# Kernel tuning notes

Measured on AMD Instinct MI355X. Metric: run time of the kernel, lower is better.

Reference implementation:

```python
import jax, jax.numpy as jnp
import numpy as np

B, S, H = 32, 2048, 1024

def setup_inputs() -> dict:
    key = jax.random.key(0)
    ks = jax.random.split(key, 8)
    sc = 1.0 / np.sqrt(H)
    return {
        "decoder_hidden": jax.random.normal(ks[0], (B, H), jnp.float32),
        "encoder_outputs": jax.random.normal(ks[1], (B, S, H), jnp.float32),
        "mask": jax.random.randint(ks[2], (B, S), 0, 2, jnp.int32),
        "Wa_w": jax.random.normal(ks[3], (H, H), jnp.float32) * sc,
        "Wa_b": jax.random.normal(ks[4], (H,), jnp.float32) * sc,
        "Ua_w": jax.random.normal(ks[5], (H, H), jnp.float32) * sc,
        "Ua_b": jax.random.normal(ks[6], (H,), jnp.float32) * sc,
        "Va_w": jax.random.normal(ks[7], (H,), jnp.float32) * sc,
        "Va_b": jnp.float32(0.0),
    }

def reference(decoder_hidden, encoder_outputs, mask, Wa_w, Wa_b, Ua_w, Ua_b, Va_w, Va_b):
    # dec proj: [B,H] -> [B,1,H]; enc proj: [B,S,H]
    dec_proj = (decoder_hidden @ Wa_w + Wa_b)[:, None, :]
    enc_proj = jnp.einsum('bsh,hk->bsk', encoder_outputs, Ua_w) + Ua_b
    energy = jnp.tanh(dec_proj + enc_proj)                      # [B,S,H]
    scores = jnp.einsum('bsh,h->bs', energy, Va_w) + Va_b       # [B,S]
    scores = jnp.where(mask == 0, jnp.float32(-1e9), scores)
    return jax.nn.softmax(scores, axis=1)
```

## Files before the change

### kernel.cpp

```cpp
#include <hip/hip_runtime.h>
#include <math.h>

#define BB 32
#define SS 2048
#define HH 1024
#define MT (BB*SS)

#define BM 256
#define BN 256
#define BK 32
#define NT (HH/BK)
#define NCH (HH/BN)
#define THREADS 512
#define BTILE 16384

typedef float  f32x4 __attribute__((ext_vector_type(4)));
typedef short  s16x8 __attribute__((ext_vector_type(8)));
typedef unsigned short u16;

__device__ inline void split1(float x, u16& h, u16& l) {
    unsigned u = __float_as_uint(x);
    h = (u16)(u >> 16);
    float hf = __uint_as_float((u >> 16) << 16);
    l = (u16)(__float_as_uint(x - hf) >> 16);
}
__device__ inline void split8v(float4 v0, float4 v1, s16x8& h, s16x8& l) {
    float x[8] = {v0.x,v0.y,v0.z,v0.w,v1.x,v1.y,v1.z,v1.w};
    #pragma unroll
    for (int j = 0; j < 8; ++j) {
        u16 hh, ll; split1(x[j], hh, ll);
        h[j] = (short)hh; l[j] = (short)ll;
    }
}

__device__ __forceinline__ void gload16(const u16* g, u16* l) {
    __builtin_amdgcn_global_load_lds(
        (const __attribute__((address_space(1))) unsigned int*)g,
        (__attribute__((address_space(3))) unsigned int*)l, 16, 0, 0);
}

__global__ void dec_proj_kernel(const float* __restrict__ dh,
                                const float* __restrict__ Wa_w,
                                const float* __restrict__ Wa_b,
                                const float* __restrict__ Ua_b,
                                float* __restrict__ dec_proj) {
    __shared__ float sdh[HH];
    const int b   = blockIdx.x;
    const int nq  = blockIdx.y;
    const int tid = threadIdx.x;
    for (int i = tid; i < HH; i += 256) sdh[i] = dh[b*HH + i];
    __syncthreads();
    const int n = nq*256 + tid;
    float acc = Wa_b[n] + Ua_b[n];
    for (int k = 0; k < HH; ++k)
        acc = fmaf(sdh[k], Wa_w[(size_t)k*HH + n], acc);
    dec_proj[b*HH + n] = acc;
}

__global__ void transpose_convert_kernel(const float* __restrict__ Ua,
                                         u16* __restrict__ B_pre) {
    __shared__ u16 shh[64][72], shl[64][72];
    const int nb = blockIdx.x * 64, kb = blockIdx.y * 64;
    const int tid = threadIdx.x;
    const int kl = tid >> 4, nl4 = (tid & 15) * 4;
    #pragma unroll
    for (int q = 0; q < 4; ++q) {
        const int k = kl + q*16;
        float4 v = *(const float4*)&Ua[(size_t)(kb + k)*HH + nb + nl4];
        float x[4] = {v.x, v.y, v.z, v.w};
        #pragma unroll
        for (int j = 0; j < 4; ++j) {
            u16 hh, ll; split1(x[j], hh, ll);
            shh[k][nl4 + j] = hh; shl[k][nl4 + j] = ll;
        }
    }
    __syncthreads();
    const int nl = tid >> 3, kc8 = (tid & 7) * 8;
    #pragma unroll
    for (int q = 0; q < 2; ++q) {
        const int n = nb + nl + q*32;
        const int kglob = kb + kc8;
        s16x8 hv, lv;
        #pragma unroll
        for (int j = 0; j < 8; ++j) {
            hv[j] = (short)shh[kc8 + j][nl + q*32];
            lv[j] = (short)shl[kc8 + j][nl + q*32];
        }
        const int nchI = n >> 8, fI = (n >> 4) & 15, lrI = n & 15;
        const int ktI = kglob >> 5, cI = (kglob >> 3) & 3;
        const size_t base = (size_t)(nchI*32 + ktI) * BTILE;
        const size_t idxH = base + fI*512 + (cI*16 + lrI)*8;
        *(s16x8*)&B_pre[idxH]        = hv;
        *(s16x8*)&B_pre[idxH + 8192] = lv;
    }
}

__global__ __launch_bounds__(THREADS, 1)
void gemm_fr_kernel(const float* __restrict__ A,
                    const u16* __restrict__ B_pre,
                    const float* __restrict__ dec_proj,
                    const float* __restrict__ Va_w,
                    float* __restrict__ partials)
{
    __shared__ __align__(16) u16 AhS[2][BM*BK];
    __shared__ __align__(16) u16 AlS[2][BM*BK];
    __shared__ __align__(16) u16 BS[2][BTILE];

    const int bid = blockIdx.x;
    const int wg  = (bid & 7) * 128 + (bid >> 3);
    const int nch = wg & 3;
    const int mt  = wg >> 2;
    const int m0  = mt * BM, n0 = nch * BN;

    const int tid = threadIdx.x, lane = tid & 63, wid = tid >> 6;
    const int wm = wid >> 2, wn = wid & 3;
    const int lr = lane & 15, lk = lane >> 4;

    const int srow = tid >> 1, shalf = tid & 1;
    const float* Ab = A + (size_t)(m0 + srow)*HH + shalf*16;
    const int awoff0 = (srow>>4)*512 + (shalf*2    )*128 + (srow&15)*8;
    const int awoff1 = (srow>>4)*512 + (shalf*2 + 1)*128 + (srow&15)*8;
    const u16* Btile = B_pre + (size_t)nch*NT*BTILE + wid*2048 + lane*8;

    f32x4 acc[8][4];
    #pragma unroll
    for (int i = 0; i < 8; ++i)
        #pragma unroll
        for (int j = 0; j < 4; ++j) acc[i][j] = (f32x4){0.f,0.f,0.f,0.f};

    s16x8  bh[4], bl[4];
    float4 a0_, a1_, a2_, a3_;

    auto gloadB = [&](int kt, int db) {
        const u16* src = Btile + (size_t)kt*BTILE;
        u16* dst = &BS[db][wid*2048];
        gload16(src,        dst);
        gload16(src +  512, dst +  512);
        gload16(src + 1024, dst + 1024);
        gload16(src + 1536, dst + 1536);
    };
    auto loadA = [&](int kt) {
        const float* p = Ab + kt*BK;
        a0_ = *(const float4*)(p + 0);
        a1_ = *(const float4*)(p + 4);
        a2_ = *(const float4*)(p + 8);
        a3_ = *(const float4*)(p + 12);
    };
    auto writeA = [&](int db) {
        s16x8 h, l;
        split8v(a0_, a1_, h, l);
        *(s16x8*)&AhS[db][awoff0] = h; *(s16x8*)&AlS[db][awoff0] = l;
        split8v(a2_, a3_, h, l);
        *(s16x8*)&AhS[db][awoff1] = h; *(s16x8*)&AlS[db][awoff1] = l;
    };
    auto readB = [&](int cb) {
        #pragma unroll
        for (int j = 0; j < 4; ++j) {
            const int off = (wn*4 + j)*512 + lane*8;
            bh[j] = *(const s16x8*)&BS[cb][off];
            bl[j] = *(const s16x8*)&BS[cb][8192 + off];
        }
    };

    loadA(0);
    gloadB(0, 0);
    writeA(0);
    __syncthreads();
    loadA(1);

    for (int j = 0; j < NT; ++j) {
        const int cb = j & 1;
        const bool hn = (j + 1 < NT);
        if (hn) gloadB(j + 1, cb ^ 1);
        __builtin_amdgcn_sched_barrier(0);

        readB(cb);
        s16x8 ahp[2], alp[2];
        {   const int o = (wm*8 + 0)*512 + lane*8;
            ahp[0] = *(const s16x8*)&AhS[cb][o];
            alp[0] = *(const s16x8*)&AlS[cb][o]; }
        #pragma unroll
        for (int f = 0; f < 8; ++f) {
            if (f < 7) {
                const int o = (wm*8 + f + 1)*512 + lane*8;
                ahp[(f+1)&1] = *(const s16x8*)&AhS[cb][o];
                alp[(f+1)&1] = *(const s16x8*)&AlS[cb][o];
            }
            const s16x8 ah = ahp[f&1], al = alp[f&1];
            __builtin_amdgcn_s_setprio(1);
            #pragma unroll
            for (int q = 0; q < 4; ++q) {
                f32x4 c = acc[f][q];
                c = __builtin_amdgcn_mfma_f32_16x16x32_bf16(ah, bh[q], c, 0, 0, 0);
                c = __builtin_amdgcn_mfma_f32_16x16x32_bf16(ah, bl[q], c, 0, 0, 0);
                c = __builtin_amdgcn_mfma_f32_16x16x32_bf16(al, bh[q], c, 0, 0, 0);
                acc[f][q] = c;
            }
            __builtin_amdgcn_s_setprio(0);
        }
        if (hn) {
            writeA(cb ^ 1);
            loadA(j + 2 < NT ? j + 2 : j + 1);
        }
        __syncthreads();
    }

    const int bidx = m0 >> 11;
    float dp[4], va[4];
    #pragma unroll
    for (int j = 0; j < 4; ++j) {
        const int n = n0 + wn*64 + j*16 + lr;
        dp[j] = dec_proj[bidx*HH + n];
        va[j] = Va_w[n];
    }
    #pragma unroll
    for (int i = 0; i < 8; ++i) {
        #pragma unroll
        for (int r = 0; r < 4; ++r) {
            float s = 0.f;
            #pragma unroll
            for (int j = 0; j < 4; ++j)
                s += va[j] * tanhf(acc[i][j][r] + dp[j]);
            s += __shfl_xor(s, 1, 64);
            s += __shfl_xor(s, 2, 64);
            s += __shfl_xor(s, 4, 64);
            s += __shfl_xor(s, 8, 64);
            if (lr == 0) {
                const int m = m0 + wm*128 + i*16 + lk*4 + r;
                partials[(size_t)m*16 + nch*4 + wn] = s;
            }
        }
    }
}

__global__ void softmax_kernel(const float* __restrict__ partials,
                               const int* __restrict__ mask,
                               const float* __restrict__ vb_ptr,
                               float* __restrict__ out)
{
    const int b   = blockIdx.x;
    const int tid = threadIdx.x;
    __shared__ float sred[8];
    const float vb = vb_ptr[0];
    float sc[8];
    float mymax = -INFINITY;
    #pragma unroll
    for (int i = 0; i < 8; ++i) {
        const int s = i*256 + tid;
        const float4* p = (const float4*)&partials[((size_t)b*SS + s)*16];
        const float4 x = p[0], y = p[1], z = p[2], w = p[3];
        float v = (((x.x+x.y)+(x.z+x.w)) + ((y.x+y.y)+(y.z+y.w)))
                + (((z.x+z.y)+(z.z+z.w)) + ((w.x+w.y)+(w.z+w.w))) + vb;
        if (mask[b*SS + s] == 0) v = -1e9f;
        sc[i] = v;
        mymax = fmaxf(mymax, v);
    }
    #pragma unroll
    for (int off = 1; off < 64; off <<= 1)
        mymax = fmaxf(mymax, __shfl_xor(mymax, off, 64));
    const int wave = tid >> 6, lane = tid & 63;
    if (lane == 0) sred[wave] = mymax;
    __syncthreads();
    const float bmax = fmaxf(fmaxf(sred[0], sred[1]), fmaxf(sred[2], sred[3]));
    float ex[8], mysum = 0.f;
    #pragma unroll
    for (int i = 0; i < 8; ++i) {
        ex[i] = __expf(sc[i] - bmax);
        mysum += ex[i];
    }
    #pragma unroll
    for (int off = 1; off < 64; off <<= 1)
        mysum += __shfl_xor(mysum, off, 64);
    if (lane == 0) sred[4 + wave] = mysum;
    __syncthreads();
    const float inv = 1.f / (sred[4] + sred[5] + sred[6] + sred[7]);
    #pragma unroll
    for (int i = 0; i < 8; ++i)
        out[(size_t)b*SS + i*256 + tid] = ex[i] * inv;
}

extern "C" void kernel_launch(void* const* d_in, const int* in_sizes, int n_in,
                              void* d_out, int out_size, void* d_ws, size_t ws_size,
                              hipStream_t stream) {
    const float* dh   = (const float*)d_in[0];
    const float* enc  = (const float*)d_in[1];
    const int*   mask = (const int*)d_in[2];
    const float* Wa_w = (const float*)d_in[3];
    const float* Wa_b = (const float*)d_in[4];
    const float* Ua_w = (const float*)d_in[5];
    const float* Ua_b = (const float*)d_in[6];
    const float* Va_w = (const float*)d_in[7];
    const float* Va_b = (const float*)d_in[8];
    float* out = (float*)d_out;

    float* dec_proj = (float*)d_ws;
    float* partials = dec_proj + BB*HH;
    u16*   B_pre    = (u16*)(partials + (size_t)MT*16);

    dec_proj_kernel<<<dim3(BB, 4), 256, 0, stream>>>(dh, Wa_w, Wa_b, Ua_b, dec_proj);
    transpose_convert_kernel<<<dim3(HH/64, HH/64), 256, 0, stream>>>(Ua_w, B_pre);
    gemm_fr_kernel<<<(MT/BM)*NCH, THREADS, 0, stream>>>(enc, B_pre, dec_proj, Va_w, partials);
    softmax_kernel<<<BB, 256, 0, stream>>>(partials, mask, Va_b, out);
}
```

Baseline: 418.7 us.

## Switch GEMM to 32x32x16 bf16 MFMA with matching LDS fragment layouts

Replaces the 16x16x32 bf16 MFMA tiling with 32x32x16 MFMA instructions and re-lays out the pre-split B buffer and the A shared-memory staging to match 32-wide fragments. The per-wave work is now 4x2 tiles of 32x32 with two k-substeps, and the epilogue reduction now spans 32 lanes. The larger MFMA shape is meant to cut the number of instructions issued and the LDS fragment reads per FLOP. In exchange the row-to-lane mapping and the accumulator layout are more involved, which raises the risk of indexing mistakes and of LDS bank conflicts.

```diff
diff --git a/kernel.cpp b/kernel.cpp
--- a/kernel.cpp
+++ b/kernel.cpp
@@ -14,8 +14,8 @@
 #define THREADS 512
 #define BTILE 16384
 
-typedef float  f32x4 __attribute__((ext_vector_type(4)));
-typedef short  s16x8 __attribute__((ext_vector_type(8)));
+typedef float  f32x16 __attribute__((ext_vector_type(16)));
+typedef short  s16x8  __attribute__((ext_vector_type(8)));
 typedef unsigned short u16;
 
 __device__ inline void split1(float x, u16& h, u16& l) {
@@ -86,10 +86,10 @@
             hv[j] = (short)shh[kc8 + j][nl + q*32];
             lv[j] = (short)shl[kc8 + j][nl + q*32];
         }
-        const int nchI = n >> 8, fI = (n >> 4) & 15, lrI = n & 15;
-        const int ktI = kglob >> 5, cI = (kglob >> 3) & 3;
-        const size_t base = (size_t)(nchI*32 + ktI) * BTILE;
-        const size_t idxH = base + fI*512 + (cI*16 + lrI)*8;
+        const int nchI = n >> 8, nfI = (n >> 5) & 7, colr = n & 31;
+        const int ktI = kglob >> 5, ksI = (kglob >> 4) & 1, chI = (kglob >> 3) & 1;
+        const size_t base = (size_t)(nchI*NT + ktI) * BTILE;
+        const size_t idxH = base + nfI*1024 + ksI*512 + colr*16 + chI*8;
         *(s16x8*)&B_pre[idxH]        = hv;
         *(s16x8*)&B_pre[idxH + 8192] = lv;
     }
@@ -114,21 +114,26 @@
 
     const int tid = threadIdx.x, lane = tid & 63, wid = tid >> 6;
     const int wm = wid >> 2, wn = wid & 3;
-    const int lr = lane & 15, lk = lane >> 4;
-
-    const int srow = tid >> 1, shalf = tid & 1;
-    const float* Ab = A + (size_t)(m0 + srow)*HH + shalf*16;
-    const int awoff0 = (srow>>4)*512 + (shalf*2    )*128 + (srow&15)*8;
-    const int awoff1 = (srow>>4)*512 + (shalf*2 + 1)*128 + (srow&15)*8;
+    const int lc = lane & 31, lh = lane >> 5;
+
+    const int e0 = tid, e1 = tid + 512;
+    const float* Ab0 = A + (size_t)(m0 + (e0>>7)*32 + ((e0>>1)&31))*HH
+                         + ((e0>>6)&1)*16 + (e0&1)*8;
+    const float* Ab1 = A + (size_t)(m0 + (e1>>7)*32 + ((e1>>1)&31))*HH
+                         + ((e1>>6)&1)*16 + (e1&1)*8;
+    const int aw0 = tid*8, aw1 = tid*8 + 4096;
     const u16* Btile = B_pre + (size_t)nch*NT*BTILE + wid*2048 + lane*8;
-
-    f32x4 acc[8][4];
-    #pragma unroll
-    for (int i = 0; i < 8; ++i)
-        #pragma unroll
-        for (int j = 0; j < 4; ++j) acc[i][j] = (f32x4){0.f,0.f,0.f,0.f};
-
-    s16x8  bh[4], bl[4];
+    const int laneoff = lc*16 + lh*8;
+
+    f32x16 acc[4][2];
+    #pragma unroll
+    for (int i = 0; i < 4; ++i)
+        #pragma unroll
+        for (int j = 0; j < 2; ++j)
+            #pragma unroll
+            for (int r = 0; r < 16; ++r) acc[i][j][r] = 0.f;
+
+    s16x8  bh[2][2], bl[2][2];
     float4 a0_, a1_, a2_, a3_;
 
     auto gloadB = [&](int kt, int db) {
@@ -140,26 +145,29 @@
         gload16(src + 1536, dst + 1536);
     };
     auto loadA = [&](int kt) {
-        const float* p = Ab + kt*BK;
-        a0_ = *(const float4*)(p + 0);
-        a1_ = *(const float4*)(p + 4);
-        a2_ = *(const float4*)(p + 8);
-        a3_ = *(const float4*)(p + 12);
+        const float* p0 = Ab0 + kt*BK;
+        const float* p1 = Ab1 + kt*BK;
+        a0_ = *(const float4*)(p0 + 0);
+        a1_ = *(const float4*)(p0 + 4);
+        a2_ = *(const float4*)(p1 + 0);
+        a3_ = *(const float4*)(p1 + 4);
     };
     auto writeA = [&](int db) {
         s16x8 h, l;
         split8v(a0_, a1_, h, l);
-        *(s16x8*)&AhS[db][awoff0] = h; *(s16x8*)&AlS[db][awoff0] = l;
+        *(s16x8*)&AhS[db][aw0] = h; *(s16x8*)&AlS[db][aw0] = l;
         split8v(a2_, a3_, h, l);
-        *(s16x8*)&AhS[db][awoff1] = h; *(s16x8*)&AlS[db][awoff1] = l;
+        *(s16x8*)&AhS[db][aw1] = h; *(s16x8*)&AlS[db][aw1] = l;
     };
     auto readB = [&](int cb) {
         #pragma unroll
-        for (int j = 0; j < 4; ++j) {
-            const int off = (wn*4 + j)*512 + lane*8;
-            bh[j] = *(const s16x8*)&BS[cb][off];
-            bl[j] = *(const s16x8*)&BS[cb][8192 + off];
-        }
+        for (int nf = 0; nf < 2; ++nf)
+            #pragma unroll
+            for (int ks = 0; ks < 2; ++ks) {
+                const int off = (wn*2 + nf)*1024 + ks*512 + laneoff;
+                bh[nf][ks] = *(const s16x8*)&BS[cb][off];
+                bl[nf][ks] = *(const s16x8*)&BS[cb][8192 + off];
+            }
     };
 
     loadA(0);
@@ -175,26 +183,34 @@
         __builtin_amdgcn_sched_barrier(0);
 
         readB(cb);
-        s16x8 ahp[2], alp[2];
-        {   const int o = (wm*8 + 0)*512 + lane*8;
-            ahp[0] = *(const s16x8*)&AhS[cb][o];
-            alp[0] = *(const s16x8*)&AlS[cb][o]; }
-        #pragma unroll
-        for (int f = 0; f < 8; ++f) {
-            if (f < 7) {
-                const int o = (wm*8 + f + 1)*512 + lane*8;
-                ahp[(f+1)&1] = *(const s16x8*)&AhS[cb][o];
-                alp[(f+1)&1] = *(const s16x8*)&AlS[cb][o];
+        s16x8 ahp[2][2], alp[2][2];
+        #pragma unroll
+        for (int ks = 0; ks < 2; ++ks) {
+            const int o = (wm*4 + 0)*1024 + ks*512 + laneoff;
+            ahp[0][ks] = *(const s16x8*)&AhS[cb][o];
+            alp[0][ks] = *(const s16x8*)&AlS[cb][o];
+        }
+        #pragma unroll
+        for (int mf = 0; mf < 4; ++mf) {
+            if (mf < 3) {
+                #pragma unroll
+                for (int ks = 0; ks < 2; ++ks) {
+                    const int o = (wm*4 + mf + 1)*1024 + ks*512 + laneoff;
+                    ahp[(mf+1)&1][ks] = *(const s16x8*)&AhS[cb][o];
+                    alp[(mf+1)&1][ks] = *(const s16x8*)&AlS[cb][o];
+                }
             }
-            const s16x8 ah = ahp[f&1], al = alp[f&1];
             __builtin_amdgcn_s_setprio(1);
             #pragma unroll
-            for (int q = 0; q < 4; ++q) {
-                f32x4 c = acc[f][q];
-                c = __builtin_amdgcn_mfma_f32_16x16x32_bf16(ah, bh[q], c, 0, 0, 0);
-                c = __builtin_amdgcn_mfma_f32_16x16x32_bf16(ah, bl[q], c, 0, 0, 0);
-                c = __builtin_amdgcn_mfma_f32_16x16x32_bf16(al, bh[q], c, 0, 0, 0);
-                acc[f][q] = c;
+            for (int nf = 0; nf < 2; ++nf) {
+                f32x16 c = acc[mf][nf];
+                #pragma unroll
+                for (int ks = 0; ks < 2; ++ks) {
+                    c = __builtin_amdgcn_mfma_f32_32x32x16_bf16(ahp[mf&1][ks], bh[nf][ks], c, 0, 0, 0);
+                    c = __builtin_amdgcn_mfma_f32_32x32x16_bf16(ahp[mf&1][ks], bl[nf][ks], c, 0, 0, 0);
+                    c = __builtin_amdgcn_mfma_f32_32x32x16_bf16(alp[mf&1][ks], bh[nf][ks], c, 0, 0, 0);
+                }
+                acc[mf][nf] = c;
             }
             __builtin_amdgcn_s_setprio(0);
         }
@@ -206,27 +222,26 @@
     }
 
     const int bidx = m0 >> 11;
-    float dp[4], va[4];
-    #pragma unroll
-    for (int j = 0; j < 4; ++j) {
-        const int n = n0 + wn*64 + j*16 + lr;
-        dp[j] = dec_proj[bidx*HH + n];
-        va[j] = Va_w[n];
-    }
-    #pragma unroll
-    for (int i = 0; i < 8; ++i) {
-        #pragma unroll
-        for (int r = 0; r < 4; ++r) {
-            float s = 0.f;
-            #pragma unroll
-            for (int j = 0; j < 4; ++j)
-                s += va[j] * tanhf(acc[i][j][r] + dp[j]);
+    float dp2[2], va2[2];
+    #pragma unroll
+    for (int nf = 0; nf < 2; ++nf) {
+        const int n = n0 + wn*64 + nf*32 + lc;
+        dp2[nf] = dec_proj[bidx*HH + n];
+        va2[nf] = Va_w[n];
+    }
+    #pragma unroll
+    for (int mf = 0; mf < 4; ++mf) {
+        #pragma unroll
+        for (int r = 0; r < 16; ++r) {
+            float s = va2[0] * tanhf(acc[mf][0][r] + dp2[0])
+                    + va2[1] * tanhf(acc[mf][1][r] + dp2[1]);
             s += __shfl_xor(s, 1, 64);
             s += __shfl_xor(s, 2, 64);
             s += __shfl_xor(s, 4, 64);
             s += __shfl_xor(s, 8, 64);
-            if (lr == 0) {
-                const int m = m0 + wm*128 + i*16 + lk*4 + r;
+            s += __shfl_xor(s, 16, 64);
+            if (lc == 0) {
+                const int m = m0 + wm*128 + mf*32 + (r & 3) + 8*(r >> 2) + 4*lh;
                 partials[(size_t)m*16 + nch*4 + wn] = s;
             }
         }
```

Result: slower. 476.6 us (+13.8%).

## Double GEMM block to 1024 threads with smaller per-wave tiles

Applied to the files above, without the earlier changes.

Splits the 256x256 output tile over 16 waves instead of 8, so each wave accumulates a 64x64 sub-tile rather than 128x64. Each thread now loads and bf16-splits half as much A and B per K step, and the per-wave accumulator shrinks. The intent is more waves in flight to hide LDS and global-memory latency. The cost is less operand reuse per wave, a tighter per-thread register budget under the new launch bounds, and the loss of the register double-buffering of A fragments inside the inner loop.

```diff
diff --git a/kernel.cpp b/kernel.cpp
--- a/kernel.cpp
+++ b/kernel.cpp
@@ -11,7 +11,7 @@
 #define BK 32
 #define NT (HH/BK)
 #define NCH (HH/BN)
-#define THREADS 512
+#define THREADS 1024
 #define BTILE 16384
 
 typedef float  f32x4 __attribute__((ext_vector_type(4)));
@@ -88,14 +88,14 @@
         }
         const int nchI = n >> 8, fI = (n >> 4) & 15, lrI = n & 15;
         const int ktI = kglob >> 5, cI = (kglob >> 3) & 3;
-        const size_t base = (size_t)(nchI*32 + ktI) * BTILE;
+        const size_t base = (size_t)(nchI*NT + ktI) * BTILE;
         const size_t idxH = base + fI*512 + (cI*16 + lrI)*8;
         *(s16x8*)&B_pre[idxH]        = hv;
         *(s16x8*)&B_pre[idxH + 8192] = lv;
     }
 }
 
-__global__ __launch_bounds__(THREADS, 1)
+__global__ __launch_bounds__(THREADS, 4)
 void gemm_fr_kernel(const float* __restrict__ A,
                     const u16* __restrict__ B_pre,
                     const float* __restrict__ dec_proj,
@@ -116,42 +116,36 @@
     const int wm = wid >> 2, wn = wid & 3;
     const int lr = lane & 15, lk = lane >> 4;
 
-    const int srow = tid >> 1, shalf = tid & 1;
-    const float* Ab = A + (size_t)(m0 + srow)*HH + shalf*16;
-    const int awoff0 = (srow>>4)*512 + (shalf*2    )*128 + (srow&15)*8;
-    const int awoff1 = (srow>>4)*512 + (shalf*2 + 1)*128 + (srow&15)*8;
-    const u16* Btile = B_pre + (size_t)nch*NT*BTILE + wid*2048 + lane*8;
-
-    f32x4 acc[8][4];
-    #pragma unroll
-    for (int i = 0; i < 8; ++i)
+    const int srow = tid >> 2, sq = tid & 3;
+    const float* Ab = A + (size_t)(m0 + srow)*HH + sq*8;
+    const int awoff = (srow >> 4)*512 + sq*128 + (srow & 15)*8;
+    const u16* Btile = B_pre + (size_t)nch*NT*BTILE + wid*1024 + lane*8;
+
+    f32x4 acc[4][4];
+    #pragma unroll
+    for (int i = 0; i < 4; ++i)
         #pragma unroll
         for (int j = 0; j < 4; ++j) acc[i][j] = (f32x4){0.f,0.f,0.f,0.f};
 
     s16x8  bh[4], bl[4];
-    float4 a0_, a1_, a2_, a3_;
+    float4 a0_, a1_;
 
     auto gloadB = [&](int kt, int db) {
         const u16* src = Btile + (size_t)kt*BTILE;
-        u16* dst = &BS[db][wid*2048];
-        gload16(src,        dst);
-        gload16(src +  512, dst +  512);
-        gload16(src + 1024, dst + 1024);
-        gload16(src + 1536, dst + 1536);
+        u16* dst = &BS[db][wid*1024];
+        gload16(src,       dst);
+        gload16(src + 512, dst + 512);
     };
     auto loadA = [&](int kt) {
         const float* p = Ab + kt*BK;
         a0_ = *(const float4*)(p + 0);
         a1_ = *(const float4*)(p + 4);
-        a2_ = *(const float4*)(p + 8);
-        a3_ = *(const float4*)(p + 12);
     };
     auto writeA = [&](int db) {
         s16x8 h, l;
         split8v(a0_, a1_, h, l);
-        *(s16x8*)&AhS[db][awoff0] = h; *(s16x8*)&AlS[db][awoff0] = l;
-        split8v(a2_, a3_, h, l);
-        *(s16x8*)&AhS[db][awoff1] = h; *(s16x8*)&AlS[db][awoff1] = l;
+        *(s16x8*)&AhS[db][awoff] = h;
+        *(s16x8*)&AlS[db][awoff] = l;
     };
     auto readB = [&](int cb) {
         #pragma unroll
@@ -175,18 +169,11 @@
         __builtin_amdgcn_sched_barrier(0);
 
         readB(cb);
-        s16x8 ahp[2], alp[2];
-        {   const int o = (wm*8 + 0)*512 + lane*8;
-            ahp[0] = *(const s16x8*)&AhS[cb][o];
-            alp[0] = *(const s16x8*)&AlS[cb][o]; }
-        #pragma unroll
-        for (int f = 0; f < 8; ++f) {
-            if (f < 7) {
-                const int o = (wm*8 + f + 1)*512 + lane*8;
-                ahp[(f+1)&1] = *(const s16x8*)&AhS[cb][o];
-                alp[(f+1)&1] = *(const s16x8*)&AlS[cb][o];
-            }
-            const s16x8 ah = ahp[f&1], al = alp[f&1];
+        #pragma unroll
+        for (int f = 0; f < 4; ++f) {
+            const int o = (wm*4 + f)*512 + lane*8;
+            const s16x8 ah = *(const s16x8*)&AhS[cb][o];
+            const s16x8 al = *(const s16x8*)&AlS[cb][o];
             __builtin_amdgcn_s_setprio(1);
             #pragma unroll
             for (int q = 0; q < 4; ++q) {
@@ -214,19 +201,19 @@
         va[j] = Va_w[n];
     }
     #pragma unroll
-    for (int i = 0; i < 8; ++i) {
+    for (int f = 0; f < 4; ++f) {
         #pragma unroll
         for (int r = 0; r < 4; ++r) {
             float s = 0.f;
             #pragma unroll
             for (int j = 0; j < 4; ++j)
-                s += va[j] * tanhf(acc[i][j][r] + dp[j]);
+                s += va[j] * tanhf(acc[f][j][r] + dp[j]);
             s += __shfl_xor(s, 1, 64);
             s += __shfl_xor(s, 2, 64);
             s += __shfl_xor(s, 4, 64);
             s += __shfl_xor(s, 8, 64);
             if (lr == 0) {
-                const int m = m0 + wm*128 + i*16 + lk*4 + r;
+                const int m = m0 + wm*64 + f*16 + lk*4 + r;
                 partials[(size_t)m*16 + nch*4 + wn] = s;
             }
         }
```

Result: faster. 392.7 us (-6.2%).
